# Kernel tuning notes

Hardware: AMD Instinct MI355X
Metric: run time of the kernel (lower is better)

Reference implementation:

```python
import jax, jax.numpy as jnp
import numpy as np

D_MODEL = 1024

def setup_inputs() -> dict:
    key = jax.random.key(0)
    ks = jax.random.split(key, 5)
    s = 1.0 / np.sqrt(D_MODEL)  # torch Linear default init scale-ish
    x = jax.random.normal(ks[0], (4, 2048, D_MODEL), dtype=jnp.float32)
    Wq = jax.random.normal(ks[1], (D_MODEL, D_MODEL), dtype=jnp.float32) * s
    Wk = jax.random.normal(ks[2], (D_MODEL, D_MODEL), dtype=jnp.float32) * s
    Wv = jax.random.normal(ks[3], (D_MODEL, D_MODEL), dtype=jnp.float32) * s
    Wo = jax.random.normal(ks[4], (D_MODEL, D_MODEL), dtype=jnp.float32) * s
    z = jnp.zeros((D_MODEL,), dtype=jnp.float32)
    return {"x": x, "Wq": Wq, "bq": z, "Wk": Wk, "bk": z, "Wv": Wv, "bv": z, "Wo": Wo, "bo": z}

def reference(x, Wq, bq, Wk, bk, Wv, bv, Wo, bo):
    # x: (B, S, D). Single-head causal attention, dropout in eval mode (identity).
    B, S, D = x.shape
    Q = jnp.einsum('bsd,ed->bse', x, Wq) + bq
    K = jnp.einsum('bsd,ed->bse', x, Wk) + bk
    V = jnp.einsum('bsd,ed->bse', x, Wv) + bv
    scores = jnp.einsum('bqd,bkd->bqk', Q, K) / jnp.sqrt(jnp.float32(D))
    causal = jnp.tril(jnp.ones((S, S), dtype=bool))  # (S, S)
    scores = jnp.where(causal, scores, -jnp.inf)
    weights = jax.nn.softmax(scores, axis=-1)
    attended = jnp.einsum('bqk,bkd->bqd', weights, V)
    out = jnp.einsum('bsd,ed->bse', attended, Wo) + bo
    return out
```

## Files before the change

kernel.cpp:

```cpp
#include <hip/hip_runtime.h>
#include <cstdint>
#include <cstddef>


#define D_MODEL 1024
#define SEQ     2048
#define BATCH   4

typedef unsigned short u16;
typedef __bf16 bf16_t;
typedef bf16_t bf16x8 __attribute__((ext_vector_type(8)));
typedef float  f32x4  __attribute__((ext_vector_type(4)));
typedef u16    u16x4  __attribute__((ext_vector_type(4)));

__device__ __forceinline__ u16 f2bf(float x) {
  union { float f; uint32_t u; } v; v.f = x;
  uint32_t r = v.u + 0x7fffu + ((v.u >> 16) & 1u);
  return (u16)(r >> 16);
}
__device__ __forceinline__ float bf2f(u16 h) {
  union { uint32_t u; float f; } v; v.u = (uint32_t)h << 16;
  return v.f;
}

__device__ __forceinline__ void gload_lds16(const u16* g, u16* l) {
  __builtin_amdgcn_global_load_lds((__attribute__((address_space(1))) void*)g,
                                   (__attribute__((address_space(3))) void*)l,
                                   16, 0, 0);
}

__device__ __forceinline__ void gemm_core(const u16* __restrict__ Ablk,
                                          const u16* __restrict__ Bblk,
                                          int lda, int ldb, int ksteps32,
                                          u16* As, u16* Bs,
                                          f32x4 acc[4][4]) {
  const int tid  = threadIdx.x;
  const int lane = tid & 63;
  const int wave = tid >> 6;
  const int wr = (wave >> 1) * 64, wc = (wave & 1) * 64;
  const int frow = lane & 15, kc = lane >> 4;
  const int ch0 = tid, ch1 = 256 + tid;
  const int m0 = ch0 >> 2, k80 = (((ch0 & 3) ^ ((m0 >> 1) & 3))) * 8;
  const int m1 = ch1 >> 2, k81 = (((ch1 & 3) ^ ((m1 >> 1) & 3))) * 8;
  int aoff[4], boff[4];
#pragma unroll
  for (int i = 0; i < 4; ++i) {
    const int ra = wr + i * 16 + frow;
    aoff[i] = (ra * 4 + (kc ^ ((ra >> 1) & 3))) * 8;
    const int rb = wc + i * 16 + frow;
    boff[i] = (rb * 4 + (kc ^ ((rb >> 1) & 3))) * 8;
  }
  for (int kt = 0; kt < ksteps32; ++kt) {
    __syncthreads();
    const int kb = kt * 32;
    gload_lds16(Ablk + (size_t)m0 * lda + kb + k80, As + ch0 * 8);
    gload_lds16(Ablk + (size_t)m1 * lda + kb + k81, As + ch1 * 8);
    gload_lds16(Bblk + (size_t)m0 * ldb + kb + k80, Bs + ch0 * 8);
    gload_lds16(Bblk + (size_t)m1 * ldb + kb + k81, Bs + ch1 * 8);
    asm volatile("s_waitcnt vmcnt(0)" ::: "memory");
    __syncthreads();

    bf16x8 af[4], bf[4];
#pragma unroll
    for (int i = 0; i < 4; ++i) af[i] = *(const bf16x8*)(As + aoff[i]);
#pragma unroll
    for (int j = 0; j < 4; ++j) bf[j] = *(const bf16x8*)(Bs + boff[j]);
#pragma unroll
    for (int i = 0; i < 4; ++i)
#pragma unroll
      for (int j = 0; j < 4; ++j)
        acc[i][j] = __builtin_amdgcn_mfma_f32_16x16x32_bf16(af[i], bf[j], acc[i][j], 0, 0, 0);
  }
}

__global__ __launch_bounds__(256) void prep_kernel(const float4* __restrict__ x,
                                                   const float4* __restrict__ wq,
                                                   const float4* __restrict__ wk,
                                                   const float4* __restrict__ wv,
                                                   const float4* __restrict__ wo,
                                                   const float* __restrict__ wv32,
                                                   u16* __restrict__ dst,
                                                   u16* __restrict__ wvt,
                                                   float* __restrict__ rssum) {
  const int blk = blockIdx.x, tid = threadIdx.x;
  if (blk < 3072) {
#pragma unroll
    for (int g = 0; g < 4; ++g) {
      const int i = (g * 3072 + blk) * 256 + tid;
      float4 v;
      bool store = true;
      if (i < 2097152) {
        v = x[i];
      } else {
        const int j = i - 2097152;
        const int w = j >> 18;
        if (w == 2) { store = false; }
        else {
          const float4* s = (w == 0) ? wq : (w == 1) ? wk : wo;
          v = s[j & 262143];
        }
      }
      if (store) {
        u16x4 o = {f2bf(v.x), f2bf(v.y), f2bf(v.z), f2bf(v.w)};
        *(u16x4*)(dst + (size_t)i * 4) = o;
      }
    }
  } else if (blk < 4096) {
    __shared__ u16 tile[32][33];
    const int tb = blk - 3072;
    const int r0 = (tb >> 5) * 32, c0 = (tb & 31) * 32;
    const int tx = tid & 31, ty = tid >> 5;
#pragma unroll
    for (int r = 0; r < 4; ++r)
      tile[ty + r * 8][tx] = f2bf(wv32[(size_t)(r0 + ty + r * 8) * D_MODEL + c0 + tx]);
    __syncthreads();
#pragma unroll
    for (int r = 0; r < 4; ++r)
      wvt[(size_t)(c0 + ty + r * 8) * D_MODEL + r0 + tx] = tile[tx][ty + r * 8];
  } else {
    f32x4* p = (f32x4*)rssum;
#pragma unroll
    for (int k = 0; k < 8; ++k) {
      f32x4 z = {0.f, 0.f, 0.f, 0.f};
      p[k * 256 + tid] = z;
    }
  }
}

__global__ __launch_bounds__(256) void stageA_kernel(
    const u16* __restrict__ xb,
    const u16* __restrict__ WqB, const u16* __restrict__ WkB,
    const u16* __restrict__ WoB, const u16* __restrict__ WvT,
    const float* __restrict__ Wo32, const float* __restrict__ bv,
    const float* __restrict__ bq, const float* __restrict__ bk,
    u16* __restrict__ Qb, u16* __restrict__ Kb,
    u16* __restrict__ Wp, float* __restrict__ bp) {
  __shared__ __align__(16) u16 As[4096];
  __shared__ __align__(16) u16 Bs[4096];
  const int blk = blockIdx.x;
  const int lane = threadIdx.x & 63, wave = threadIdx.x >> 6;
  const int wr = (wave >> 1) * 64, wc = (wave & 1) * 64;
  const int cl = lane & 15, rl = (lane >> 4) * 4;

  if (blk < 64) {
    const int f0 = (blk >> 3) * 128, e0 = (blk & 7) * 128;
    f32x4 acc[4][4] = {};
    gemm_core(WoB + (size_t)f0 * D_MODEL, WvT + (size_t)e0 * D_MODEL,
              D_MODEL, D_MODEL, 32, As, Bs, acc);
#pragma unroll
    for (int j = 0; j < 4; ++j) {
      const int col = e0 + wc + j * 16 + cl;
#pragma unroll
      for (int i = 0; i < 4; ++i)
#pragma unroll
        for (int r = 0; r < 4; ++r) {
          const int row = f0 + wr + i * 16 + rl + r;
          Wp[(size_t)row * D_MODEL + col] = f2bf(acc[i][j][r]);
        }
    }
  } else if (blk < 80) {
    const int f = (blk - 64) * 64 + (threadIdx.x >> 2);
    const int dq = threadIdx.x & 3;
    const float* row = Wo32 + (size_t)f * D_MODEL + dq * 256;
    const float* bvq = bv + dq * 256;
    float s = 0.f;
#pragma unroll 8
    for (int i = 0; i < 256; ++i) s += row[i] * bvq[i];
    s += __shfl_xor(s, 1);
    s += __shfl_xor(s, 2);
    if (dq == 0) bp[f] = s;
  } else {
    const int v = blk - 80;
    const int c = v & 7, s = v >> 3;
    const int row0 = (c * 8 + (s >> 4)) * 128;
    const int cz = s & 15;
    const int z = cz >> 3;
    const int col0 = (cz & 7) * 128;
    const u16*   W    = z ? WkB : WqB;
    const float* bias = z ? bk : bq;
    u16*         out  = z ? Kb : Qb;
    f32x4 acc[4][4] = {};
    gemm_core(xb + (size_t)row0 * D_MODEL, W + (size_t)col0 * D_MODEL,
              D_MODEL, D_MODEL, 32, As, Bs, acc);
#pragma unroll
    for (int j = 0; j < 4; ++j) {
      const int col = col0 + wc + j * 16 + cl;
      const float bb = bias[col];
#pragma unroll
      for (int i = 0; i < 4; ++i)
#pragma unroll
        for (int r = 0; r < 4; ++r) {
          const int row = row0 + wr + i * 16 + rl + r;
          out[(size_t)row * D_MODEL + col] = f2bf(acc[i][j][r] + bb);
        }
    }
  }
}

__global__ __launch_bounds__(256) void stageB_kernel(
    const u16* __restrict__ xb, const u16* __restrict__ Wp,
    const float* __restrict__ bp,
    const u16* __restrict__ Qb, const u16* __restrict__ Kb,
    u16* __restrict__ Vt, u16* __restrict__ Eb, float* __restrict__ rssum) {
  __shared__ __align__(16) u16 As[4096];
  __shared__ __align__(16) u16 Bs[4096];
  const int blk = blockIdx.x;
  const int lane = threadIdx.x & 63, wave = threadIdx.x >> 6;
  const int wr = (wave >> 1) * 64, wc = (wave & 1) * 64;
  const int cl = lane & 15, rl = (lane >> 4) * 4;

  if (blk < 544) {
    const int c = blk & 7, s = blk >> 3;
    int b, qi, ji;
    if (s < 48) {
      static const int sq_tab[6] = {1, 2, 2, 3, 3, 3};
      static const int sj_tab[6] = {0, 0, 1, 0, 1, 2};
      const int fi = c * 3 + (s >> 4);
      const int off = s & 15;
      b = fi / 6;
      const int fs = fi % 6;
      qi = sq_tab[fs] * 4 + (off >> 2);
      ji = sj_tab[fs] * 4 + (off & 3);
    } else {
      static const int di_tab[10] = {0, 1, 1, 2, 2, 2, 3, 3, 3, 3};
      static const int dj_tab[10] = {0, 0, 1, 0, 1, 2, 0, 1, 2, 3};
      const int k = (s - 48) / 10;
      const int off = (s - 48) % 10;
      const int di = c * 2 + k;
      b = di >> 2;
      const int dk = di & 3;
      qi = dk * 4 + di_tab[off];
      ji = dk * 4 + dj_tab[off];
    }
    const u16* A  = Qb + (size_t)(b * SEQ + qi * 128) * D_MODEL;
    const u16* Bt = Kb + (size_t)(b * SEQ + ji * 128) * D_MODEL;
    f32x4 acc[4][4] = {};
    gemm_core(A, Bt, D_MODEL, D_MODEL, 32, As, Bs, acc);
    u16* out = Eb + (size_t)b * SEQ * SEQ;
    float* rs = rssum + b * SEQ;
#pragma unroll
    for (int i = 0; i < 4; ++i)
#pragma unroll
      for (int r = 0; r < 4; ++r) {
        const int q = qi * 128 + wr + i * 16 + rl + r;
        float ps = 0.f;
#pragma unroll
        for (int j = 0; j < 4; ++j) {
          const int jj = ji * 128 + wc + j * 16 + cl;
          u16 h16 = (jj <= q) ? f2bf(__expf(acc[i][j][r] * 0.03125f)) : (u16)0;
          out[(size_t)q * SEQ + jj] = h16;
          ps += bf2f(h16);
        }
        ps += __shfl_xor(ps, 1);
        ps += __shfl_xor(ps, 2);
        ps += __shfl_xor(ps, 4);
        ps += __shfl_xor(ps, 8);
        if (cl == 0) atomicAdd(&rs[q], ps);
      }
  } else {
    const int v = blk - 544;
    const int c = v & 7, s = v >> 3;
    const int row0 = (c * 8 + (s >> 3)) * 128;
    const int col0 = (s & 7) * 128;
    f32x4 acc[4][4] = {};
    gemm_core(xb + (size_t)row0 * D_MODEL, Wp + (size_t)col0 * D_MODEL,
              D_MODEL, D_MODEL, 32, As, Bs, acc);
    const int b = row0 >> 11;
    u16* vt = Vt + (size_t)b * D_MODEL * SEQ;
#pragma unroll
    for (int j = 0; j < 4; ++j) {
      const int col = col0 + wc + j * 16 + cl;
      const float bb = bp[col];
#pragma unroll
      for (int i = 0; i < 4; ++i) {
        const int s0 = (row0 & 2047) + wr + i * 16 + rl;
        u16x4 o = {f2bf(acc[i][j][0] + bb), f2bf(acc[i][j][1] + bb),
                   f2bf(acc[i][j][2] + bb), f2bf(acc[i][j][3] + bb)};
        *(u16x4*)(vt + (size_t)col * SEQ + s0) = o;
      }
    }
  }
}

__global__ __launch_bounds__(256) void pv_kernel(const u16* __restrict__ Eb,
                                                 const u16* __restrict__ Vt,
                                                 const float* __restrict__ rssum,
                                                 const float* __restrict__ bo,
                                                 float* __restrict__ Out) {
  __shared__ __align__(16) u16 As[4096];
  __shared__ __align__(16) u16 Bs[4096];
  const int u = blockIdx.x;
  const int c = u & 7, s = u >> 3;
  const int b  = c >> 1;
  const int dt = (c & 1) * 4 + (s >> 4);
  const int qt = 15 - (s & 15);
  const u16* A  = Eb + (size_t)b * SEQ * SEQ + (size_t)(qt * 128) * SEQ;
  const u16* Bt = Vt + (size_t)b * D_MODEL * SEQ + (size_t)(dt * 128) * SEQ;
  f32x4 acc[4][4] = {};
  gemm_core(A, Bt, SEQ, SEQ, (qt + 1) * 4, As, Bs, acc);
  const int lane = threadIdx.x & 63, wave = threadIdx.x >> 6;
  const int wr = (wave >> 1) * 64, wc = (wave & 1) * 64;
  const int cl = lane & 15, rl = (lane >> 4) * 4;
#pragma unroll
  for (int i = 0; i < 4; ++i)
#pragma unroll
    for (int r = 0; r < 4; ++r) {
      const int row = qt * 128 + wr + i * 16 + rl + r;
      const float invl = 1.0f / rssum[b * SEQ + row];
#pragma unroll
      for (int j = 0; j < 4; ++j) {
        const int col = dt * 128 + wc + j * 16 + cl;
        Out[(size_t)(b * SEQ + row) * D_MODEL + col] = acc[i][j][r] * invl + bo[col];
      }
    }
}

extern "C" void kernel_launch(void* const* d_in, const int* in_sizes, int n_in,
                              void* d_out, int out_size, void* d_ws, size_t ws_size,
                              hipStream_t stream) {
  const float* x  = (const float*)d_in[0];
  const float* Wq = (const float*)d_in[1];
  const float* bq = (const float*)d_in[2];
  const float* Wk = (const float*)d_in[3];
  const float* bk = (const float*)d_in[4];
  const float* Wv = (const float*)d_in[5];
  const float* bv = (const float*)d_in[6];
  const float* Wo = (const float*)d_in[7];
  const float* bo = (const float*)d_in[8];
  float* out = (float*)d_out;
  char* ws = (char*)d_ws;

  u16*   xb  = (u16*)(ws);
  u16*   Wb  = (u16*)(ws + (16u << 20));
  u16*   Qb  = (u16*)(ws + (24u << 20));
  u16*   Kb  = (u16*)(ws + (40u << 20));
  u16*   Vt  = (u16*)(ws + (56u << 20));
  u16*   Eb  = (u16*)(ws + (72u << 20));
  u16*   WvT = (u16*)(ws + (104u << 20));
  u16*   Wp  = (u16*)(ws + (106u << 20));
  float* bp  = (float*)(ws + (108u << 20));
  float* rssum = (float*)(ws + (20u << 20));

  prep_kernel<<<4097, 256, 0, stream>>>((const float4*)x, (const float4*)Wq,
                                        (const float4*)Wk, (const float4*)Wv,
                                        (const float4*)Wo, Wv, xb, WvT, rssum);
  stageA_kernel<<<1104, 256, 0, stream>>>(xb, Wb, Wb + (1u << 20), Wb + (3u << 20),
                                          WvT, Wo, bv, bq, bk, Qb, Kb, Wp, bp);
  stageB_kernel<<<1056, 256, 0, stream>>>(xb, Wp, bp, Qb, Kb, Vt, Eb, rssum);
  pv_kernel<<<512, 256, 0, stream>>>(Eb, Vt, rssum, bo, out);
}
```

Measured before the change: 265.5 us.

## Split PV GEMM over key range with atomic accumulation into bias-initialized output

The PV kernel now splits each causal row tile's key range into two halves, launching twice as many blocks, which balances the triangular work and raises occupancy. Partial results are combined with float atomic adds into the output. The output is pre-filled with the bias by extra blocks in the prep kernel. This trades extra atomic traffic, an output pre-initialization pass and nondeterministic summation order for better load balance across CUs.

```diff
diff --git a/kernel.cpp b/kernel.cpp
--- a/kernel.cpp
+++ b/kernel.cpp
@@ -79,9 +79,11 @@
                                                    const float4* __restrict__ wv,
                                                    const float4* __restrict__ wo,
                                                    const float* __restrict__ wv32,
+                                                   const float* __restrict__ bo,
                                                    u16* __restrict__ dst,
                                                    u16* __restrict__ wvt,
-                                                   float* __restrict__ rssum) {
+                                                   float* __restrict__ rssum,
+                                                   float4* __restrict__ outv) {
   const int blk = blockIdx.x, tid = threadIdx.x;
   if (blk < 3072) {
 #pragma unroll
@@ -117,12 +119,20 @@
 #pragma unroll
     for (int r = 0; r < 4; ++r)
       wvt[(size_t)(c0 + ty + r * 8) * D_MODEL + r0 + tx] = tile[tx][ty + r * 8];
-  } else {
+  } else if (blk == 4096) {
     f32x4* p = (f32x4*)rssum;
 #pragma unroll
     for (int k = 0; k < 8; ++k) {
       f32x4 z = {0.f, 0.f, 0.f, 0.f};
       p[k * 256 + tid] = z;
+    }
+  } else {
+    const int ob = blk - 4097;
+    const float4* bo4 = (const float4*)bo;
+#pragma unroll
+    for (int k = 0; k < 4; ++k) {
+      const int i = ob * 1024 + k * 256 + tid;
+      outv[i] = bo4[i & 255];
     }
   }
 }
@@ -285,19 +295,24 @@
 __global__ __launch_bounds__(256) void pv_kernel(const u16* __restrict__ Eb,
                                                  const u16* __restrict__ Vt,
                                                  const float* __restrict__ rssum,
-                                                 const float* __restrict__ bo,
                                                  float* __restrict__ Out) {
   __shared__ __align__(16) u16 As[4096];
   __shared__ __align__(16) u16 Bs[4096];
   const int u = blockIdx.x;
   const int c = u & 7, s = u >> 3;
+  const int half = s >> 6, s2 = s & 63;
   const int b  = c >> 1;
-  const int dt = (c & 1) * 4 + (s >> 4);
-  const int qt = 15 - (s & 15);
-  const u16* A  = Eb + (size_t)b * SEQ * SEQ + (size_t)(qt * 128) * SEQ;
-  const u16* Bt = Vt + (size_t)b * D_MODEL * SEQ + (size_t)(dt * 128) * SEQ;
+  const int dt = (c & 1) * 4 + (s2 >> 4);
+  const int qt = 15 - (s2 & 15);
+  const int ntiles = qt + 1;
+  const int h0 = (ntiles + 1) >> 1;
+  const int t0 = half ? h0 : 0;
+  const int tn = half ? (ntiles - h0) : h0;
+  if (tn == 0) return;
+  const u16* A  = Eb + (size_t)b * SEQ * SEQ + (size_t)(qt * 128) * SEQ + t0 * 128;
+  const u16* Bt = Vt + (size_t)b * D_MODEL * SEQ + (size_t)(dt * 128) * SEQ + t0 * 128;
   f32x4 acc[4][4] = {};
-  gemm_core(A, Bt, SEQ, SEQ, (qt + 1) * 4, As, Bs, acc);
+  gemm_core(A, Bt, SEQ, SEQ, tn * 4, As, Bs, acc);
   const int lane = threadIdx.x & 63, wave = threadIdx.x >> 6;
   const int wr = (wave >> 1) * 64, wc = (wave & 1) * 64;
   const int cl = lane & 15, rl = (lane >> 4) * 4;
@@ -310,7 +325,8 @@
 #pragma unroll
       for (int j = 0; j < 4; ++j) {
         const int col = dt * 128 + wc + j * 16 + cl;
-        Out[(size_t)(b * SEQ + row) * D_MODEL + col] = acc[i][j][r] * invl + bo[col];
+        unsafeAtomicAdd(&Out[(size_t)(b * SEQ + row) * D_MODEL + col],
+                        acc[i][j][r] * invl);
       }
     }
 }
@@ -341,11 +357,12 @@
   float* bp  = (float*)(ws + (108u << 20));
   float* rssum = (float*)(ws + (20u << 20));
 
-  prep_kernel<<<4097, 256, 0, stream>>>((const float4*)x, (const float4*)Wq,
+  prep_kernel<<<6145, 256, 0, stream>>>((const float4*)x, (const float4*)Wq,
                                         (const float4*)Wk, (const float4*)Wv,
-                                        (const float4*)Wo, Wv, xb, WvT, rssum);
+                                        (const float4*)Wo, Wv, bo, xb, WvT,
+                                        rssum, (float4*)out);
   stageA_kernel<<<1104, 256, 0, stream>>>(xb, Wb, Wb + (1u << 20), Wb + (3u << 20),
                                           WvT, Wo, bv, bq, bk, Qb, Kb, Wp, bp);
   stageB_kernel<<<1056, 256, 0, stream>>>(xb, Wp, bp, Qb, Kb, Vt, Eb, rssum);
-  pv_kernel<<<512, 256, 0, stream>>>(Eb, Vt, rssum, bo, out);
-}
+  pv_kernel<<<1024, 256, 0, stream>>>(Eb, Vt, rssum, out);
+}
```

Result: slower. 287.7 us (+8.4%).
